# Kernel tuning notes

Hardware: AMD Instinct MI355X
Metric: run time of the kernel (lower is better)

Reference implementation:

```python
import jax, jax.numpy as jnp
import numpy as np

B, D, H, S = 32768, 512, 8, 3  # batch, stream_dim, heads, num_streams
DH = D // H
EPS = 1e-5


def setup_inputs() -> dict:
    key = jax.random.key(0)
    ks = jax.random.split(key, 16)
    sc = lambda fan_in: 1.0 / np.sqrt(fan_in)
    return {
        "kinematic_h": jax.random.normal(ks[0], (B, D), jnp.float32),
        "color_h": jax.random.normal(ks[1], (B, D), jnp.float32),
        "spinor_h": jax.random.normal(ks[2], (B, D), jnp.float32),
        # MultiheadAttention packed in-proj and out-proj
        "w_in": jax.random.normal(ks[3], (3 * D, D), jnp.float32) * sc(D),
        "b_in": jnp.zeros((3 * D,), jnp.float32),
        "w_out": jax.random.normal(ks[4], (D, D), jnp.float32) * sc(D),
        "b_out": jnp.zeros((D,), jnp.float32),
        # stream gate: Linear(3D -> 3) + softmax
        "w_gate": jax.random.normal(ks[5], (S, S * D), jnp.float32) * sc(S * D),
        "b_gate": jnp.zeros((S,), jnp.float32),
        # fusion MLP: Linear(3D -> 2D), SiLU, Linear(2D -> D)
        "w1": jax.random.normal(ks[6], (2 * D, S * D), jnp.float32) * sc(S * D),
        "b1": jnp.zeros((2 * D,), jnp.float32),
        "w2": jax.random.normal(ks[7], (D, 2 * D), jnp.float32) * sc(2 * D),
        "b2": jnp.zeros((D,), jnp.float32),
        # LayerNorm
        "gamma": jnp.ones((D,), jnp.float32),
        "beta": jnp.zeros((D,), jnp.float32),
    }


def reference(kinematic_h, color_h, spinor_h, w_in, b_in, w_out, b_out,
              w_gate, b_gate, w1, b1, w2, b2, gamma, beta):
    stacked = jnp.stack([kinematic_h, color_h, spinor_h], axis=1)  # [B,S,D]
    b = stacked.shape[0]
    # self-attention (Q=K=V=stacked), packed QKV projection
    qkv = stacked @ w_in.T + b_in  # [B,S,3D]
    q, k, v = jnp.split(qkv, 3, axis=-1)
    q = q.reshape(b, S, H, DH)
    k = k.reshape(b, S, H, DH)
    v = v.reshape(b, S, H, DH)
    scores = jnp.einsum("bqhd,bkhd->bhqk", q, k) / np.sqrt(DH)
    attn = jax.nn.softmax(scores, axis=-1)
    out = jnp.einsum("bhqk,bkhd->bqhd", attn, v).reshape(b, S, D)
    attn_out = stacked + (out @ w_out.T + b_out)  # residual, [B,S,D]
    # gating softmax over streams
    flat = attn_out.reshape(b, S * D)
    gates = jax.nn.softmax(flat @ w_gate.T + b_gate, axis=-1)[..., None]  # [B,S,1]
    gated = (attn_out * gates).reshape(b, S * D)
    # fusion MLP (dropout=eval no-op)
    h = jax.nn.silu(gated @ w1.T + b1)
    fused = h @ w2.T + b2  # [B,D]
    # LayerNorm
    mu = jnp.mean(fused, axis=-1, keepdims=True)
    var = jnp.var(fused, axis=-1, keepdims=True)
    return (fused - mu) * jax.lax.rsqrt(var + EPS) * gamma + beta
```

## Files before the change

### kernel.cpp

```cpp
#include <hip/hip_runtime.h>
#include <stdint.h>


typedef float f32x4 __attribute__((ext_vector_type(4)));
typedef short bf16x8 __attribute__((ext_vector_type(8)));

__device__ __forceinline__ float bf2f(unsigned short h) {
  return __uint_as_float(((unsigned)h) << 16);
}
__device__ __forceinline__ unsigned short f2bf(float f) {
  unsigned u = __float_as_uint(f);
  u += 0x7FFFu + ((u >> 16) & 1u);
  return (unsigned short)(u >> 16);
}
__device__ __forceinline__ ushort4 f2bf4(float4 v) {
  return make_ushort4(f2bf(v.x), f2bf(v.y), f2bf(v.z), f2bf(v.w));
}

__device__ __forceinline__ void async_cp16(const void* g, void* lds) {
  __builtin_amdgcn_global_load_lds(
      (const __attribute__((address_space(1))) void*)g,
      (__attribute__((address_space(3))) void*)lds, 16, 0, 0);
}

__global__ void __launch_bounds__(256) cvtbf(const float4* __restrict__ src,
                                             ushort4* __restrict__ dst, int n4) {
  int i = blockIdx.x * 256 + threadIdx.x;
  if (i < n4) dst[i] = f2bf4(src[i]);
}

__global__ void __launch_bounds__(256) pack3(const float4* __restrict__ X0,
                                             const float4* __restrict__ X1,
                                             const float4* __restrict__ X2,
                                             ushort4* __restrict__ S) {
  int tid = blockIdx.x * 256 + threadIdx.x;
  int b = tid >> 7, c = tid & 127;
  long base = (long)(3 * b) * 128 + c;
  S[base]       = f2bf4(X0[tid]);
  S[base + 128] = f2bf4(X1[tid]);
  S[base + 256] = f2bf4(X2[tid]);
}

__global__ void __launch_bounds__(256)
qkv_attn(const unsigned short* __restrict__ S,
         const unsigned short* __restrict__ Wi,
         const float* __restrict__ bin,
         unsigned short* __restrict__ AO) {
  __shared__ unsigned short lds[96 * 200];
  unsigned short* Abuf = lds;
  unsigned short* Bbuf = lds + 6144;

  const int t = threadIdx.x;
  const int lane = t & 63;
  const int wave = t >> 6;
  const int wm = wave >> 1, wn = wave & 1;

  const int ny = gridDim.y;
  const int id = blockIdx.y * 8 + blockIdx.x;
  const int xcd = id & 7, j = id >> 3;
  const int h = j & 7;
  const long m0 = (long)(xcd * (ny >> 3) + (j >> 3)) * 96;

  const int trow = t >> 3;
  const int swz = ((t & 7) ^ (trow & 7)) << 3;
  const unsigned short* Ag = S + (m0 + trow) * 512 + swz;
  const unsigned short* Bg = Wi + ((long)h * 64 + trow) * 512 + swz;
  unsigned short* AsD = Abuf + t * 8;
  unsigned short* BsD = Bbuf + t * 8;

  f32x4 acc[3][6] = {};
  const int arow0 = wm * 48 + (lane & 15);
  const int brow0 = wn * 96 + (lane & 15);

  for (int k0 = 0; k0 < 512; k0 += 64) {
    __syncthreads();
#pragma unroll
    for (int r = 0; r < 3; r++)
      async_cp16(Ag + (long)r * 32 * 512 + k0, AsD + r * 2048);
#pragma unroll
    for (int r = 0; r < 6; r++)
      async_cp16(Bg + (long)((r >> 1) * 512 + (r & 1) * 32) * 512 + k0, BsD + r * 2048);
    __syncthreads();
#pragma unroll
    for (int kk = 0; kk < 2; kk++) {
      const int sc = ((kk * 4 + (lane >> 4)) ^ (lane & 7)) << 3;
      bf16x8 af[3], bfr[6];
#pragma unroll
      for (int mt = 0; mt < 3; mt++)
        af[mt] = *(const bf16x8*)&Abuf[(arow0 + mt * 16) * 64 + sc];
#pragma unroll
      for (int nt = 0; nt < 6; nt++)
        bfr[nt] = *(const bf16x8*)&Bbuf[(brow0 + nt * 16) * 64 + sc];
#pragma unroll
      for (int mt = 0; mt < 3; mt++)
#pragma unroll
        for (int nt = 0; nt < 6; nt++)
          acc[mt][nt] = __builtin_amdgcn_mfma_f32_16x16x32_bf16(
              af[mt], bfr[nt], acc[mt][nt], 0, 0, 0);
    }
  }

  __syncthreads();
  const int crow0 = wm * 48 + ((lane >> 4) << 2);
  const int ccol0 = wn * 96 + (lane & 15);
#pragma unroll
  for (int nt = 0; nt < 6; nt++) {
    const int col = ccol0 + nt * 16;
    const float bv = bin[(col >> 6) * 512 + h * 64 + (col & 63)];
#pragma unroll
    for (int mt = 0; mt < 3; mt++)
#pragma unroll
      for (int r = 0; r < 4; r++)
        lds[(crow0 + mt * 16 + r) * 200 + col] = f2bf(acc[mt][nt][r] + bv);
  }
  __syncthreads();

  const int bi = lane >> 3;
  const int l8 = lane & 7;
  const int r0 = (wave * 8 + bi) * 3;
  float q[3][8], k[3][8], v[3][8];
#pragma unroll
  for (int s = 0; s < 3; s++) {
    const unsigned short* rowp = &lds[(r0 + s) * 200 + l8 * 8];
    uint4 qu = *(const uint4*)(rowp);
    uint4 ku = *(const uint4*)(rowp + 64);
    uint4 vu = *(const uint4*)(rowp + 128);
    const unsigned* qw = (const unsigned*)&qu;
    const unsigned* kw = (const unsigned*)&ku;
    const unsigned* vw = (const unsigned*)&vu;
#pragma unroll
    for (int jj = 0; jj < 4; jj++) {
      q[s][2 * jj]     = __uint_as_float(qw[jj] << 16);
      q[s][2 * jj + 1] = __uint_as_float(qw[jj] & 0xffff0000u);
      k[s][2 * jj]     = __uint_as_float(kw[jj] << 16);
      k[s][2 * jj + 1] = __uint_as_float(kw[jj] & 0xffff0000u);
      v[s][2 * jj]     = __uint_as_float(vw[jj] << 16);
      v[s][2 * jj + 1] = __uint_as_float(vw[jj] & 0xffff0000u);
    }
  }
  float p[3][3];
#pragma unroll
  for (int s = 0; s < 3; s++)
#pragma unroll
    for (int u = 0; u < 3; u++) {
      float d = 0.f;
#pragma unroll
      for (int e = 0; e < 8; e++) d = fmaf(q[s][e], k[u][e], d);
      p[s][u] = d;
    }
#pragma unroll
  for (int m = 1; m < 8; m <<= 1)
#pragma unroll
    for (int s = 0; s < 3; s++)
#pragma unroll
      for (int u = 0; u < 3; u++) p[s][u] += __shfl_xor(p[s][u], m, 64);

  unsigned short* ob = AO + (m0 + r0) * 512 + h * 64 + l8 * 8;
#pragma unroll
  for (int s = 0; s < 3; s++) {
    float a0 = p[s][0] * 0.125f, a1 = p[s][1] * 0.125f, a2 = p[s][2] * 0.125f;
    float mx = fmaxf(a0, fmaxf(a1, a2));
    float e0 = __expf(a0 - mx), e1 = __expf(a1 - mx), e2 = __expf(a2 - mx);
    float inv = 1.0f / (e0 + e1 + e2);
    unsigned ow[4];
#pragma unroll
    for (int jj = 0; jj < 4; jj++) {
      float lo = (e0 * v[0][2 * jj] + e1 * v[1][2 * jj] + e2 * v[2][2 * jj]) * inv;
      float hi = (e0 * v[0][2 * jj + 1] + e1 * v[1][2 * jj + 1] + e2 * v[2][2 * jj + 1]) * inv;
      ow[jj] = (unsigned)f2bf(lo) | ((unsigned)f2bf(hi) << 16);
    }
    *(uint4*)(ob + s * 512) = *(uint4*)ow;
  }
}

enum { EPI_BF16 = 0, EPI_RES = 1, EPI_SILU = 2, EPI_F32 = 3 };

template <int EPI>
__global__ void __launch_bounds__(256)
gemm_bt(const unsigned short* __restrict__ A,
        const unsigned short* __restrict__ W,
        const float* __restrict__ bias,
        const unsigned short* __restrict__ Res,
        void* __restrict__ Out,
        int K, int N) {
  __shared__ unsigned short As[128 * 64];
  __shared__ unsigned short Bs[128 * 64];
  const int t = threadIdx.x;
  const int lane = t & 63;
  const int wave = t >> 6;
  const int wm = wave >> 1, wn = wave & 1;

  const int nb = gridDim.x;
  const int nblocks = nb * gridDim.y;
  const int id = blockIdx.y * nb + blockIdx.x;
  const int lid = ((nblocks & 7) == 0) ? ((id & 7) * (nblocks >> 3) + (id >> 3)) : id;
  const long bm = (long)(lid / nb) * 128;
  const long bn = (long)(lid % nb) * 128;

  const int srow = t >> 3;
  const int schunk = ((t & 7) ^ (srow & 7)) << 3;
  const unsigned short* Ag = A + (bm + srow) * (long)K + schunk;
  const unsigned short* Wg = W + (bn + srow) * (long)K + schunk;
  unsigned short* AsD = As + t * 8;
  unsigned short* BsD = Bs + t * 8;

  f32x4 acc[4][4] = {};
  const int arow0 = wm * 64 + (lane & 15);
  const int brow0 = wn * 64 + (lane & 15);

  for (int k0 = 0; k0 < K; k0 += 64) {
    __syncthreads();
#pragma unroll
    for (int i = 0; i < 4; i++) {
      async_cp16(Ag + (long)(i * 32) * K + k0, AsD + i * 2048);
      async_cp16(Wg + (long)(i * 32) * K + k0, BsD + i * 2048);
    }
    __syncthreads();
#pragma unroll
    for (int kk = 0; kk < 2; kk++) {
      const int sc = ((kk * 4 + (lane >> 4)) ^ (lane & 7)) << 3;
      bf16x8 af[4], bfr[4];
#pragma unroll
      for (int mt = 0; mt < 4; mt++)
        af[mt] = *(const bf16x8*)&As[(arow0 + mt * 16) * 64 + sc];
#pragma unroll
      for (int nt = 0; nt < 4; nt++)
        bfr[nt] = *(const bf16x8*)&Bs[(brow0 + nt * 16) * 64 + sc];
#pragma unroll
      for (int mt = 0; mt < 4; mt++)
#pragma unroll
        for (int nt = 0; nt < 4; nt++)
          acc[mt][nt] = __builtin_amdgcn_mfma_f32_16x16x32_bf16(
              af[mt], bfr[nt], acc[mt][nt], 0, 0, 0);
    }
  }

  const long row0 = bm + wm * 64 + ((lane >> 4) << 2);
  const int col0 = (int)bn + wn * 64 + (lane & 15);
#pragma unroll
  for (int nt = 0; nt < 4; nt++) {
    const int col = col0 + nt * 16;
    const float bv = bias[col];
#pragma unroll
    for (int mt = 0; mt < 4; mt++) {
      const long rbase = row0 + mt * 16;
#pragma unroll
      for (int r = 0; r < 4; r++) {
        float v = acc[mt][nt][r] + bv;
        const long idx = (rbase + r) * (long)N + col;
        if (EPI == EPI_RES) v += bf2f(Res[idx]);
        if (EPI == EPI_SILU) v = v * (1.0f / (1.0f + __expf(-v)));
        if (EPI == EPI_F32)
          ((float*)Out)[idx] = v;
        else
          ((unsigned short*)Out)[idx] = f2bf(v);
      }
    }
  }
}

__global__ void __launch_bounds__(256) gate3(const unsigned short* AT,
                                             const float* __restrict__ WG,
                                             const float* __restrict__ BG,
                                             unsigned short* G) {
  int row = blockIdx.x * 4 + (threadIdx.x >> 6);
  int lane = threadIdx.x & 63;
  const unsigned short* rp = AT + (long)row * 1536 + lane * 8;
  float x[3][8];
  float p[3] = {0.f, 0.f, 0.f};
#pragma unroll
  for (int seg = 0; seg < 3; seg++) {
    uint4 u = *(const uint4*)(rp + seg * 512);
    const unsigned* uw = (const unsigned*)&u;
#pragma unroll
    for (int j = 0; j < 4; j++) {
      x[seg][2 * j]     = __uint_as_float(uw[j] << 16);
      x[seg][2 * j + 1] = __uint_as_float(uw[j] & 0xffff0000u);
    }
    const int e0 = seg * 512 + lane * 8;
#pragma unroll
    for (int g = 0; g < 3; g++) {
      const float* wp = WG + g * 1536 + e0;
#pragma unroll
      for (int e = 0; e < 8; e++) p[g] = fmaf(x[seg][e], wp[e], p[g]);
    }
  }
#pragma unroll
  for (int m = 1; m < 64; m <<= 1)
#pragma unroll
    for (int g = 0; g < 3; g++) p[g] += __shfl_xor(p[g], m, 64);
  float g0 = p[0] + BG[0], g1 = p[1] + BG[1], g2 = p[2] + BG[2];
  float mx = fmaxf(g0, fmaxf(g1, g2));
  g0 = __expf(g0 - mx); g1 = __expf(g1 - mx); g2 = __expf(g2 - mx);
  float inv = 1.0f / (g0 + g1 + g2);
  float gs[3] = {g0 * inv, g1 * inv, g2 * inv};
  unsigned short* op = G + (long)row * 1536 + lane * 8;
#pragma unroll
  for (int seg = 0; seg < 3; seg++) {
    unsigned ow[4];
#pragma unroll
    for (int j = 0; j < 4; j++)
      ow[j] = (unsigned)f2bf(x[seg][2 * j] * gs[seg]) |
              ((unsigned)f2bf(x[seg][2 * j + 1] * gs[seg]) << 16);
    *(uint4*)(op + seg * 512) = *(uint4*)ow;
  }
}

__global__ void __launch_bounds__(256) lnorm(const float* __restrict__ F,
                                             const float* __restrict__ gamma,
                                             const float* __restrict__ beta,
                                             float* __restrict__ out) {
  int row = blockIdx.x * 4 + (threadIdx.x >> 6);
  int lane = threadIdx.x & 63;
  const float4* fr = (const float4*)(F + (long)row * 512);
  float4 a = fr[lane], c = fr[lane + 64];
  float s = a.x + a.y + a.z + a.w + c.x + c.y + c.z + c.w;
  float ss = a.x * a.x + a.y * a.y + a.z * a.z + a.w * a.w +
             c.x * c.x + c.y * c.y + c.z * c.z + c.w * c.w;
#pragma unroll
  for (int m = 1; m < 64; m <<= 1) {
    s += __shfl_xor(s, m, 64);
    ss += __shfl_xor(ss, m, 64);
  }
  float mean = s * (1.0f / 512.0f);
  float var = ss * (1.0f / 512.0f) - mean * mean;
  float rstd = rsqrtf(var + 1e-5f);
  const float4* g4 = (const float4*)gamma;
  const float4* b4 = (const float4*)beta;
  float4 g0 = g4[lane], g1 = g4[lane + 64], be0 = b4[lane], be1 = b4[lane + 64];
  float4 o0, o1;
  o0.x = (a.x - mean) * rstd * g0.x + be0.x;
  o0.y = (a.y - mean) * rstd * g0.y + be0.y;
  o0.z = (a.z - mean) * rstd * g0.z + be0.z;
  o0.w = (a.w - mean) * rstd * g0.w + be0.w;
  o1.x = (c.x - mean) * rstd * g1.x + be1.x;
  o1.y = (c.y - mean) * rstd * g1.y + be1.y;
  o1.z = (c.z - mean) * rstd * g1.z + be1.z;
  o1.w = (c.w - mean) * rstd * g1.w + be1.w;
  float4* orow = (float4*)(out + (long)row * 512);
  orow[lane] = o0;
  orow[lane + 64] = o1;
}

extern "C" void kernel_launch(void* const* d_in, const int* in_sizes, int n_in,
                              void* d_out, int out_size, void* d_ws, size_t ws_size,
                              hipStream_t stream) {
  const float* kin    = (const float*)d_in[0];
  const float* colr   = (const float*)d_in[1];
  const float* spi    = (const float*)d_in[2];
  const float* w_in   = (const float*)d_in[3];
  const float* b_in   = (const float*)d_in[4];
  const float* w_out  = (const float*)d_in[5];
  const float* b_out  = (const float*)d_in[6];
  const float* w_gate = (const float*)d_in[7];
  const float* b_gate = (const float*)d_in[8];
  const float* w1     = (const float*)d_in[9];
  const float* b1     = (const float*)d_in[10];
  const float* w2     = (const float*)d_in[11];
  const float* b2     = (const float*)d_in[12];
  const float* gamma  = (const float*)d_in[13];
  const float* beta   = (const float*)d_in[14];
  float* out = (float*)d_out;

  long Bc = 32768;
  while (Bc > 1024 && (size_t)(6291456 + 9216 * Bc) > ws_size) Bc >>= 1;
  const int nch = (int)(32768 / Bc);

  char* ws = (char*)d_ws;
  unsigned short* Wic = (unsigned short*)(ws);
  unsigned short* Woc = (unsigned short*)(ws + 1572864);
  unsigned short* W1c = (unsigned short*)(ws + 2097152);
  unsigned short* W2c = (unsigned short*)(ws + 5242880);
  char* Sb  = ws + 6291456;
  char* AOb = Sb + 3072 * Bc;
  char* ATb = AOb + 3072 * Bc;

  cvtbf<<<768, 256, 0, stream>>>((const float4*)w_in, (ushort4*)Wic, 196608);
  cvtbf<<<256, 256, 0, stream>>>((const float4*)w_out, (ushort4*)Woc, 65536);
  cvtbf<<<1536, 256, 0, stream>>>((const float4*)w1, (ushort4*)W1c, 393216);
  cvtbf<<<512, 256, 0, stream>>>((const float4*)w2, (ushort4*)W2c, 131072);

  for (int c = 0; c < nch; c++) {
    const long boff = (long)c * Bc;
    unsigned short* S_c  = (unsigned short*)Sb;
    unsigned short* AO_c = (unsigned short*)AOb;
    unsigned short* AT_c = (unsigned short*)ATb;
    unsigned short* G_c  = AT_c;
    unsigned short* H_c  = (unsigned short*)AOb;
    float*          F_c  = (float*)Sb;

    pack3<<<(int)(Bc / 2), 256, 0, stream>>>(
        (const float4*)(kin + boff * 512), (const float4*)(colr + boff * 512),
        (const float4*)(spi + boff * 512), (ushort4*)S_c);
    qkv_attn<<<dim3(8, (int)(Bc / 32)), 256, 0, stream>>>(S_c, Wic, b_in, AO_c);
    gemm_bt<EPI_RES><<<dim3(4, (int)(3 * Bc / 128)), 256, 0, stream>>>(
        AO_c, Woc, b_out, S_c, AT_c, 512, 512);
    gate3<<<(int)(Bc / 4), 256, 0, stream>>>(AT_c, w_gate, b_gate, G_c);
    gemm_bt<EPI_SILU><<<dim3(8, (int)(Bc / 128)), 256, 0, stream>>>(
        G_c, W1c, b1, nullptr, H_c, 1536, 1024);
    gemm_bt<EPI_F32><<<dim3(4, (int)(Bc / 128)), 256, 0, stream>>>(
        H_c, W2c, b2, nullptr, F_c, 1024, 512);
    lnorm<<<(int)(Bc / 4), 256, 0, stream>>>(F_c, gamma, beta, out + boff * 512);
  }
}
```

Baseline: 794.8 us.

## Fuse out-projection with stream gating, and second MLP GEMM with LayerNorm

Replaces the residual out-projection GEMM plus separate gate kernel with one kernel. Each block computes full 512-wide rows for 16 batch elements (48 stream rows), reduces the gate logits in LDS, applies the softmax gate and writes the gated bf16 activations in place over the stacked input. The W2 GEMM likewise computes full output rows per block and applies LayerNorm in its epilogue, removing the fp32 intermediate and the lnorm pass. This saves global round trips and workspace, but each block must restream the whole weight matrix, and the epilogues use scalar strided stores.

```diff
diff --git a/kernel.cpp b/kernel.cpp
--- a/kernel.cpp
+++ b/kernel.cpp
@@ -171,6 +171,216 @@
     }
     *(uint4*)(ob + s * 512) = *(uint4*)ow;
   }
+}
+
+__global__ void __launch_bounds__(256)
+proj_gate(const unsigned short* __restrict__ AO,
+          const unsigned short* Sres,
+          const unsigned short* __restrict__ Wo,
+          const float* __restrict__ bo,
+          const float* __restrict__ WG,
+          const float* __restrict__ BG,
+          unsigned short* G) {
+  __shared__ unsigned short Bs[512 * 32];
+  __shared__ float gpart[48][4][3];
+  __shared__ float gates[16][3];
+  const int t = threadIdx.x;
+  const int lane = t & 63;
+  const int w = t >> 6;
+  const long m0 = (long)blockIdx.x * 48;
+  const int ar = lane & 15, aq = lane >> 4;
+
+  f32x4 acc[3][8] = {};
+  for (int k0 = 0; k0 < 512; k0 += 32) {
+    __syncthreads();
+#pragma unroll
+    for (int i = 0; i < 8; i++) {
+      const int c = i * 256 + t;
+      const int row = c >> 2, slot = c & 3;
+      const int chunk = slot ^ ((row >> 1) & 3);
+      async_cp16(Wo + row * 512 + k0 + chunk * 8, Bs + c * 8);
+    }
+    bf16x8 af[3];
+#pragma unroll
+    for (int mt = 0; mt < 3; mt++)
+      af[mt] = *(const bf16x8*)(AO + (m0 + mt * 16 + ar) * 512 + k0 + aq * 8);
+    __syncthreads();
+    bf16x8 bfr[8];
+#pragma unroll
+    for (int nt = 0; nt < 8; nt++) {
+      const int br = w * 128 + nt * 16 + ar;
+      bfr[nt] = *(const bf16x8*)&Bs[br * 32 + ((aq ^ ((br >> 1) & 3)) << 3)];
+    }
+#pragma unroll
+    for (int mt = 0; mt < 3; mt++)
+#pragma unroll
+      for (int nt = 0; nt < 8; nt++)
+        acc[mt][nt] = __builtin_amdgcn_mfma_f32_16x16x32_bf16(
+            af[mt], bfr[nt], acc[mt][nt], 0, 0, 0);
+  }
+
+#pragma unroll
+  for (int nt = 0; nt < 8; nt++) {
+    const int col = w * 128 + nt * 16 + ar;
+    const float bv = bo[col];
+#pragma unroll
+    for (int mt = 0; mt < 3; mt++)
+#pragma unroll
+      for (int r = 0; r < 4; r++) {
+        const int crow = mt * 16 + aq * 4 + r;
+        acc[mt][nt][r] += bv + bf2f(Sres[(m0 + crow) * 512 + col]);
+      }
+  }
+#pragma unroll
+  for (int mt = 0; mt < 3; mt++)
+#pragma unroll
+    for (int r = 0; r < 4; r++) {
+      const int crow = mt * 16 + aq * 4 + r;
+      const int s = crow % 3;
+      float p0 = 0.f, p1 = 0.f, p2 = 0.f;
+#pragma unroll
+      for (int nt = 0; nt < 8; nt++) {
+        const int col = w * 128 + nt * 16 + ar;
+        const float vv = acc[mt][nt][r];
+        const float* wg = WG + s * 512 + col;
+        p0 = fmaf(vv, wg[0], p0);
+        p1 = fmaf(vv, wg[1536], p1);
+        p2 = fmaf(vv, wg[3072], p2);
+      }
+#pragma unroll
+      for (int msk = 1; msk < 16; msk <<= 1) {
+        p0 += __shfl_xor(p0, msk, 64);
+        p1 += __shfl_xor(p1, msk, 64);
+        p2 += __shfl_xor(p2, msk, 64);
+      }
+      if (ar == 0) {
+        gpart[crow][w][0] = p0; gpart[crow][w][1] = p1; gpart[crow][w][2] = p2;
+      }
+    }
+  __syncthreads();
+  if (t < 16) {
+    float l0 = BG[0], l1 = BG[1], l2 = BG[2];
+    for (int s = 0; s < 3; s++)
+      for (int ww = 0; ww < 4; ww++) {
+        l0 += gpart[t * 3 + s][ww][0];
+        l1 += gpart[t * 3 + s][ww][1];
+        l2 += gpart[t * 3 + s][ww][2];
+      }
+    float mx = fmaxf(l0, fmaxf(l1, l2));
+    l0 = __expf(l0 - mx); l1 = __expf(l1 - mx); l2 = __expf(l2 - mx);
+    float inv = 1.0f / (l0 + l1 + l2);
+    gates[t][0] = l0 * inv; gates[t][1] = l1 * inv; gates[t][2] = l2 * inv;
+  }
+  __syncthreads();
+#pragma unroll
+  for (int mt = 0; mt < 3; mt++)
+#pragma unroll
+    for (int r = 0; r < 4; r++) {
+      const int crow = mt * 16 + aq * 4 + r;
+      const float gv = gates[crow / 3][crow % 3];
+#pragma unroll
+      for (int nt = 0; nt < 8; nt++) {
+        const int col = w * 128 + nt * 16 + ar;
+        G[(m0 + crow) * 512 + col] = f2bf(acc[mt][nt][r] * gv);
+      }
+    }
+}
+
+__global__ void __launch_bounds__(512)
+mlp2_ln(const unsigned short* __restrict__ H,
+        const unsigned short* __restrict__ W2,
+        const float* __restrict__ b2,
+        const float* __restrict__ gamma,
+        const float* __restrict__ beta,
+        float* __restrict__ out) {
+  __shared__ unsigned short Bs[512 * 32];
+  __shared__ float stats[64][4][2];
+  __shared__ float mv[64][2];
+  const int t = threadIdx.x;
+  const int lane = t & 63;
+  const int w = t >> 6;
+  const int wm = w >> 2, wn = w & 3;
+  const long m0 = (long)blockIdx.x * 64;
+  const int ar = lane & 15, aq = lane >> 4;
+
+  f32x4 acc[2][8] = {};
+  for (int k0 = 0; k0 < 1024; k0 += 32) {
+    __syncthreads();
+#pragma unroll
+    for (int i = 0; i < 4; i++) {
+      const int c = i * 512 + t;
+      const int row = c >> 2, slot = c & 3;
+      const int chunk = slot ^ ((row >> 1) & 3);
+      async_cp16(W2 + row * 1024 + k0 + chunk * 8, Bs + c * 8);
+    }
+    bf16x8 af[2];
+#pragma unroll
+    for (int mt = 0; mt < 2; mt++)
+      af[mt] = *(const bf16x8*)(H + (m0 + wm * 32 + mt * 16 + ar) * 1024 + k0 + aq * 8);
+    __syncthreads();
+    bf16x8 bfr[8];
+#pragma unroll
+    for (int nt = 0; nt < 8; nt++) {
+      const int br = wn * 128 + nt * 16 + ar;
+      bfr[nt] = *(const bf16x8*)&Bs[br * 32 + ((aq ^ ((br >> 1) & 3)) << 3)];
+    }
+#pragma unroll
+    for (int mt = 0; mt < 2; mt++)
+#pragma unroll
+      for (int nt = 0; nt < 8; nt++)
+        acc[mt][nt] = __builtin_amdgcn_mfma_f32_16x16x32_bf16(
+            af[mt], bfr[nt], acc[mt][nt], 0, 0, 0);
+  }
+
+#pragma unroll
+  for (int nt = 0; nt < 8; nt++) {
+    const float bv = b2[wn * 128 + nt * 16 + ar];
+#pragma unroll
+    for (int mt = 0; mt < 2; mt++)
+#pragma unroll
+      for (int r = 0; r < 4; r++) acc[mt][nt][r] += bv;
+  }
+#pragma unroll
+  for (int mt = 0; mt < 2; mt++)
+#pragma unroll
+    for (int r = 0; r < 4; r++) {
+      const int crow = wm * 32 + mt * 16 + aq * 4 + r;
+      float s = 0.f, ss = 0.f;
+#pragma unroll
+      for (int nt = 0; nt < 8; nt++) {
+        const float vv = acc[mt][nt][r];
+        s += vv; ss = fmaf(vv, vv, ss);
+      }
+#pragma unroll
+      for (int msk = 1; msk < 16; msk <<= 1) {
+        s += __shfl_xor(s, msk, 64);
+        ss += __shfl_xor(ss, msk, 64);
+      }
+      if (ar == 0) { stats[crow][wn][0] = s; stats[crow][wn][1] = ss; }
+    }
+  __syncthreads();
+  if (t < 64) {
+    float s = stats[t][0][0] + stats[t][1][0] + stats[t][2][0] + stats[t][3][0];
+    float ss = stats[t][0][1] + stats[t][1][1] + stats[t][2][1] + stats[t][3][1];
+    float mean = s * (1.0f / 512.0f);
+    float var = ss * (1.0f / 512.0f) - mean * mean;
+    mv[t][0] = mean;
+    mv[t][1] = rsqrtf(var + 1e-5f);
+  }
+  __syncthreads();
+#pragma unroll
+  for (int mt = 0; mt < 2; mt++)
+#pragma unroll
+    for (int r = 0; r < 4; r++) {
+      const int crow = wm * 32 + mt * 16 + aq * 4 + r;
+      const float mean = mv[crow][0], rstd = mv[crow][1];
+#pragma unroll
+      for (int nt = 0; nt < 8; nt++) {
+        const int col = wn * 128 + nt * 16 + ar;
+        out[(m0 + crow) * 512 + col] =
+            (acc[mt][nt][r] - mean) * rstd * gamma[col] + beta[col];
+      }
+    }
 }
 
 enum { EPI_BF16 = 0, EPI_RES = 1, EPI_SILU = 2, EPI_F32 = 3 };
@@ -257,89 +467,6 @@
       }
     }
   }
-}
-
-__global__ void __launch_bounds__(256) gate3(const unsigned short* AT,
-                                             const float* __restrict__ WG,
-                                             const float* __restrict__ BG,
-                                             unsigned short* G) {
-  int row = blockIdx.x * 4 + (threadIdx.x >> 6);
-  int lane = threadIdx.x & 63;
-  const unsigned short* rp = AT + (long)row * 1536 + lane * 8;
-  float x[3][8];
-  float p[3] = {0.f, 0.f, 0.f};
-#pragma unroll
-  for (int seg = 0; seg < 3; seg++) {
-    uint4 u = *(const uint4*)(rp + seg * 512);
-    const unsigned* uw = (const unsigned*)&u;
-#pragma unroll
-    for (int j = 0; j < 4; j++) {
-      x[seg][2 * j]     = __uint_as_float(uw[j] << 16);
-      x[seg][2 * j + 1] = __uint_as_float(uw[j] & 0xffff0000u);
-    }
-    const int e0 = seg * 512 + lane * 8;
-#pragma unroll
-    for (int g = 0; g < 3; g++) {
-      const float* wp = WG + g * 1536 + e0;
-#pragma unroll
-      for (int e = 0; e < 8; e++) p[g] = fmaf(x[seg][e], wp[e], p[g]);
-    }
-  }
-#pragma unroll
-  for (int m = 1; m < 64; m <<= 1)
-#pragma unroll
-    for (int g = 0; g < 3; g++) p[g] += __shfl_xor(p[g], m, 64);
-  float g0 = p[0] + BG[0], g1 = p[1] + BG[1], g2 = p[2] + BG[2];
-  float mx = fmaxf(g0, fmaxf(g1, g2));
-  g0 = __expf(g0 - mx); g1 = __expf(g1 - mx); g2 = __expf(g2 - mx);
-  float inv = 1.0f / (g0 + g1 + g2);
-  float gs[3] = {g0 * inv, g1 * inv, g2 * inv};
-  unsigned short* op = G + (long)row * 1536 + lane * 8;
-#pragma unroll
-  for (int seg = 0; seg < 3; seg++) {
-    unsigned ow[4];
-#pragma unroll
-    for (int j = 0; j < 4; j++)
-      ow[j] = (unsigned)f2bf(x[seg][2 * j] * gs[seg]) |
-              ((unsigned)f2bf(x[seg][2 * j + 1] * gs[seg]) << 16);
-    *(uint4*)(op + seg * 512) = *(uint4*)ow;
-  }
-}
-
-__global__ void __launch_bounds__(256) lnorm(const float* __restrict__ F,
-                                             const float* __restrict__ gamma,
-                                             const float* __restrict__ beta,
-                                             float* __restrict__ out) {
-  int row = blockIdx.x * 4 + (threadIdx.x >> 6);
-  int lane = threadIdx.x & 63;
-  const float4* fr = (const float4*)(F + (long)row * 512);
-  float4 a = fr[lane], c = fr[lane + 64];
-  float s = a.x + a.y + a.z + a.w + c.x + c.y + c.z + c.w;
-  float ss = a.x * a.x + a.y * a.y + a.z * a.z + a.w * a.w +
-             c.x * c.x + c.y * c.y + c.z * c.z + c.w * c.w;
-#pragma unroll
-  for (int m = 1; m < 64; m <<= 1) {
-    s += __shfl_xor(s, m, 64);
-    ss += __shfl_xor(ss, m, 64);
-  }
-  float mean = s * (1.0f / 512.0f);
-  float var = ss * (1.0f / 512.0f) - mean * mean;
-  float rstd = rsqrtf(var + 1e-5f);
-  const float4* g4 = (const float4*)gamma;
-  const float4* b4 = (const float4*)beta;
-  float4 g0 = g4[lane], g1 = g4[lane + 64], be0 = b4[lane], be1 = b4[lane + 64];
-  float4 o0, o1;
-  o0.x = (a.x - mean) * rstd * g0.x + be0.x;
-  o0.y = (a.y - mean) * rstd * g0.y + be0.y;
-  o0.z = (a.z - mean) * rstd * g0.z + be0.z;
-  o0.w = (a.w - mean) * rstd * g0.w + be0.w;
-  o1.x = (c.x - mean) * rstd * g1.x + be1.x;
-  o1.y = (c.y - mean) * rstd * g1.y + be1.y;
-  o1.z = (c.z - mean) * rstd * g1.z + be1.z;
-  o1.w = (c.w - mean) * rstd * g1.w + be1.w;
-  float4* orow = (float4*)(out + (long)row * 512);
-  orow[lane] = o0;
-  orow[lane + 64] = o1;
 }
 
 extern "C" void kernel_launch(void* const* d_in, const int* in_sizes, int n_in,
@@ -363,7 +490,7 @@
   float* out = (float*)d_out;
 
   long Bc = 32768;
-  while (Bc > 1024 && (size_t)(6291456 + 9216 * Bc) > ws_size) Bc >>= 1;
+  while (Bc > 1024 && (size_t)(6291456 + 6144 * Bc) > ws_size) Bc >>= 1;
   const int nch = (int)(32768 / Bc);
 
   char* ws = (char*)d_ws;
@@ -373,7 +500,6 @@
   unsigned short* W2c = (unsigned short*)(ws + 5242880);
   char* Sb  = ws + 6291456;
   char* AOb = Sb + 3072 * Bc;
-  char* ATb = AOb + 3072 * Bc;
 
   cvtbf<<<768, 256, 0, stream>>>((const float4*)w_in, (ushort4*)Wic, 196608);
   cvtbf<<<256, 256, 0, stream>>>((const float4*)w_out, (ushort4*)Woc, 65536);
@@ -384,22 +510,18 @@
     const long boff = (long)c * Bc;
     unsigned short* S_c  = (unsigned short*)Sb;
     unsigned short* AO_c = (unsigned short*)AOb;
-    unsigned short* AT_c = (unsigned short*)ATb;
-    unsigned short* G_c  = AT_c;
+    unsigned short* G_c  = S_c;
     unsigned short* H_c  = (unsigned short*)AOb;
-    float*          F_c  = (float*)Sb;
 
     pack3<<<(int)(Bc / 2), 256, 0, stream>>>(
         (const float4*)(kin + boff * 512), (const float4*)(colr + boff * 512),
         (const float4*)(spi + boff * 512), (ushort4*)S_c);
     qkv_attn<<<dim3(8, (int)(Bc / 32)), 256, 0, stream>>>(S_c, Wic, b_in, AO_c);
-    gemm_bt<EPI_RES><<<dim3(4, (int)(3 * Bc / 128)), 256, 0, stream>>>(
-        AO_c, Woc, b_out, S_c, AT_c, 512, 512);
-    gate3<<<(int)(Bc / 4), 256, 0, stream>>>(AT_c, w_gate, b_gate, G_c);
+    proj_gate<<<(int)(Bc / 16), 256, 0, stream>>>(AO_c, S_c, Woc, b_out,
+                                                  w_gate, b_gate, G_c);
     gemm_bt<EPI_SILU><<<dim3(8, (int)(Bc / 128)), 256, 0, stream>>>(
         G_c, W1c, b1, nullptr, H_c, 1536, 1024);
-    gemm_bt<EPI_F32><<<dim3(4, (int)(Bc / 128)), 256, 0, stream>>>(
-        H_c, W2c, b2, nullptr, F_c, 1024, 512);
-    lnorm<<<(int)(Bc / 4), 256, 0, stream>>>(F_c, gamma, beta, out + boff * 512);
-  }
-}
+    mlp2_ln<<<(int)(Bc / 64), 512, 0, stream>>>(H_c, W2c, b2, gamma, beta,
+                                                out + boff * 512);
+  }
+}
```

After: 948.4 us. +19.3%, slower.
